# Performance work log

Hardware: AMD Instinct MI355X
Metric: run time of the kernel (lower is better)

## Reference

```python
import jax, jax.numpy as jnp
import numpy as np

LN_EPS = 1e-12
B, L, D, V, PATCH, IMG, C = 64, 40, 768, 30522, 16, 384, 3
GRID = IMG // PATCH            # 24
NPATCH = GRID * GRID           # 576


def layer_norm(x, g, b):
    m = jnp.mean(x, axis=-1, keepdims=True)
    v = jnp.var(x, axis=-1, keepdims=True)
    return (x - m) * jax.lax.rsqrt(v + LN_EPS) * g + b


def setup_inputs() -> dict:
    key = jax.random.key(0)
    ks = jax.random.split(key, 12)
    s = 0.02
    return {
        "input_ids": jax.random.randint(ks[0], (B, L), 0, V, dtype=jnp.int32),
        "attention_mask": jnp.ones((B, L), jnp.int32),
        "token_type_ids": jnp.zeros((B, L), jnp.int32),
        "pixel_values": jax.random.normal(ks[1], (B, C, IMG, IMG), jnp.float32),
        "pixel_mask": jnp.ones((B, IMG, IMG), jnp.int32),
        "word_emb": jax.random.normal(ks[2], (V, D), jnp.float32) * s,
        "text_pos_emb": jax.random.normal(ks[3], (L, D), jnp.float32) * s,
        "text_tok_emb": jax.random.normal(ks[4], (2, D), jnp.float32) * s,
        "ln_g": jnp.ones((D,), jnp.float32),
        "ln_b": jnp.zeros((D,), jnp.float32),
        "conv_w": jax.random.normal(ks[5], (D, C, PATCH, PATCH), jnp.float32) * s,
        "conv_b": jnp.zeros((D,), jnp.float32),
        "cls_token": jnp.zeros((1, 1, D), jnp.float32),
        "vis_pos_emb": jax.random.normal(ks[6], (1, NPATCH + 1, D), jnp.float32) * s,
        "mod_type_emb": jax.random.normal(ks[7], (2, D), jnp.float32) * s,
    }


def reference(input_ids, attention_mask, token_type_ids, pixel_values, pixel_mask,
              word_emb, text_pos_emb, text_tok_emb, ln_g, ln_b,
              conv_w, conv_b, cls_token, vis_pos_emb, mod_type_emb):
    # ---- text embeddings (BERT-style) ----
    te = word_emb[input_ids] + text_pos_emb[None, :, :] + text_tok_emb[token_type_ids]
    te = layer_norm(te, ln_g, ln_b)  # [B, L, D]

    # ---- visual_embed ----
    # patch projection conv (stride = patch size)
    x = jax.lax.conv_general_dilated(
        pixel_values, conv_w, window_strides=(PATCH, PATCH), padding='VALID',
        dimension_numbers=('NCHW', 'OIHW', 'NCHW')) + conv_b[None, :, None, None]
    # [B, D, 24, 24] -> [B, 576, D]
    x = x.reshape(B, D, NPATCH).transpose(0, 2, 1)
    # full pixel_mask => x_h = x_w = GRID for every sample; bilinear interp of the
    # [1, D, 24, 24] spatial pos-embed to (24, 24) with align_corners=True is identity,
    # all patches valid, valid_nums == max_image_length => selection is identity.
    pos_embed = vis_pos_emb[:, 1:, :]           # [1, NPATCH, D]
    img = x + pos_embed                          # [B, NPATCH, D]
    image_masks = jnp.ones((B, NPATCH), attention_mask.dtype)

    # ---- modality type embeddings ----
    te = te + mod_type_emb[0][None, None, :]
    img = img + mod_type_emb[1][None, None, :]

    # ---- concat with cls token ----
    emb = jnp.concatenate([te, img], axis=1)
    cls = jnp.broadcast_to(cls_token, (B, 1, D))
    emb = jnp.concatenate([cls, emb], axis=1)    # [B, 1+L+NPATCH, D]
    masks = jnp.concatenate(
        [jnp.ones((B, 1), attention_mask.dtype), attention_mask, image_masks], axis=1)
    return emb, masks
```

## Files before the change

kernel.cpp:

```cpp
#include <hip/hip_runtime.h>

typedef __attribute__((ext_vector_type(4))) float f4;
typedef __attribute__((ext_vector_type(4))) float f32x4;
typedef __attribute__((ext_vector_type(8))) __bf16 bf8;
typedef __attribute__((ext_vector_type(8))) unsigned short us8;

#define NB 64
#define LSEQ 40
#define D_DIM 768
#define NPATCH 576
#define SEQ 617
#define K_DIM 768
#define M_DIM (NB * NPATCH)
#define A_BYTES 56623104
#define GEMM_LDS 131072

static __device__ __forceinline__ unsigned short f2bf(float f) {
    union { float f; unsigned u; } v; v.f = f;
    unsigned r = v.u + 0x7FFFu + ((v.u >> 16) & 1u);
    return (unsigned short)(r >> 16);
}

static __device__ __forceinline__ void gload_lds16(const void* g, void* l) {
    __builtin_amdgcn_global_load_lds(
        (const __attribute__((address_space(1))) unsigned int*)g,
        (__attribute__((address_space(3))) unsigned int*)l,
        16, 0, 0);
}

__global__ __launch_bounds__(256) void convert_w(const float* __restrict__ w,
                                                 unsigned short* __restrict__ o) {
    int t = blockIdx.x * 256 + threadIdx.x;
    int cs = t % 96, n = t / 96;
    int blk = cs >> 3, c = cs & 7;
    int cl = (blk << 3) | (c ^ (n & 7));
    const float* s = w + (size_t)n * 768 + cl * 8;
    f4 a = *(const f4*)s;
    f4 b = *(const f4*)(s + 4);
    us8 r;
    r[0]=f2bf(a[0]); r[1]=f2bf(a[1]); r[2]=f2bf(a[2]); r[3]=f2bf(a[3]);
    r[4]=f2bf(b[0]); r[5]=f2bf(b[1]); r[6]=f2bf(b[2]); r[7]=f2bf(b[3]);
    *(us8*)(o + (size_t)n * 768 + cs * 8) = r;
}

__global__ __launch_bounds__(256) void convert_patches(const float* __restrict__ px,
                                                       unsigned short* __restrict__ A) {
    int t = blockIdx.x * 256 + threadIdx.x;
    int cs = t % 96, m = t / 96;
    int blk = cs >> 3, c = cs & 7;
    int cl = (blk << 3) | (c ^ (m & 7));
    int k = cl * 8;
    int b = m / 576, p = m % 576;
    int ph = p / 24, pw = p % 24;
    int ch = k >> 8, rr = k & 255, i = rr >> 4, j = rr & 15;
    const float* s = px + ((size_t)(b * 3 + ch) * 384 + ph * 16 + i) * 384 + pw * 16 + j;
    f4 a = *(const f4*)s;
    f4 d = *(const f4*)(s + 4);
    us8 o;
    o[0]=f2bf(a[0]); o[1]=f2bf(a[1]); o[2]=f2bf(a[2]); o[3]=f2bf(a[3]);
    o[4]=f2bf(d[0]); o[5]=f2bf(d[1]); o[6]=f2bf(d[2]); o[7]=f2bf(d[3]);
    *(us8*)(A + (size_t)m * 768 + cs * 8) = o;
}

__global__ __launch_bounds__(256) void text_kernel(
    const int* __restrict__ ids, const int* __restrict__ tti,
    const float* __restrict__ we, const float* __restrict__ pe,
    const float* __restrict__ tke, const float* __restrict__ g,
    const float* __restrict__ bb, const float* __restrict__ mod,
    float* __restrict__ out) {
    int row = blockIdx.x * 4 + (threadIdx.x >> 6);
    int lane = threadIdx.x & 63;
    int b = row / 40, l = row % 40;
    const float* wp = we + (size_t)ids[row] * 768;
    const float* pp = pe + l * 768;
    const float* tp = tke + (size_t)tti[row] * 768;
    f4 x[3];
    float s = 0.f, q = 0.f;
#pragma unroll
    for (int j = 0; j < 3; ++j) {
        int d = j * 256 + lane * 4;
        f4 v = *(const f4*)(wp + d);
        f4 v2 = *(const f4*)(pp + d);
        f4 v3 = *(const f4*)(tp + d);
        v = v + v2 + v3;
        x[j] = v;
        s += v[0] + v[1] + v[2] + v[3];
        q += v[0]*v[0] + v[1]*v[1] + v[2]*v[2] + v[3]*v[3];
    }
#pragma unroll
    for (int o = 32; o > 0; o >>= 1) { s += __shfl_xor(s, o); q += __shfl_xor(q, o); }
    float mean = s * (1.0f / 768.0f);
    float var = q * (1.0f / 768.0f) - mean * mean;
    float rstd = rsqrtf(var + 1e-12f);
    float* op = out + ((size_t)b * SEQ + 1 + l) * 768;
#pragma unroll
    for (int j = 0; j < 3; ++j) {
        int d = j * 256 + lane * 4;
        f4 gg = *(const f4*)(g + d);
        f4 bv = *(const f4*)(bb + d);
        f4 mm = *(const f4*)(mod + d);
        f4 r = (x[j] - mean) * rstd * gg + bv + mm;
        *(f4*)(op + d) = r;
    }
}

__global__ __launch_bounds__(512, 2) void gemm_patch(
    const __bf16* __restrict__ A, const __bf16* __restrict__ W,
    const float* __restrict__ conv_b, const float* __restrict__ vis_pos,
    const float* __restrict__ mod, float* __restrict__ out) {
    extern __shared__ __align__(16) char smem[];
    const int tid = threadIdx.x;
    const int w = tid >> 6, lane = tid & 63;

    int lid = blockIdx.x;
    int gwi = (lid & 7) * 54 + (lid >> 3);
    const int tile_n = (gwi % 3) * 256;
    const int tile_m = (gwi / 3) * 256;
    const int wm = w >> 2, wn = w & 3;
    const int wr = wm * 128, wc = wn * 64;

    f32x4 acc[8][4] = {};
    const char* Ab = (const char*)A;
    const char* Bb = (const char*)W;

    auto STAGE_A = [&](int p, int kt) {
        const int k0b = kt * 128;
        char* dst = smem + p * 32768;
#pragma unroll
        for (int i = 0; i < 4; ++i) {
            int uoff = (w << 10) + i * 8192;
            int loff = uoff + (lane << 4);
            int row = loff >> 7, col = loff & 127;
            gload_lds16(Ab + (size_t)(tile_m + row) * 1536 + k0b + col, dst + uoff);
        }
    };
    auto STAGE_B = [&](int p, int kt) {
        const int k0b = kt * 128;
        char* dst = smem + 65536 + p * 32768;
#pragma unroll
        for (int i = 0; i < 4; ++i) {
            int uoff = (w << 10) + i * 8192;
            int loff = uoff + (lane << 4);
            int row = loff >> 7, col = loff & 127;
            gload_lds16(Bb + (size_t)(tile_n + row) * 1536 + k0b + col, dst + uoff);
        }
    };

    STAGE_A(0, 0);
    STAGE_B(0, 0);
    asm volatile("s_waitcnt vmcnt(0)" ::: "memory");
    __builtin_amdgcn_sched_barrier(0);
    __builtin_amdgcn_s_barrier();
    __builtin_amdgcn_sched_barrier(0);

    const int rsel = lane & 15;
    const int hk = lane >> 4;

    for (int kt = 0; kt < 12; ++kt) {
        const int p = kt & 1;
        const char* Al = smem + p * 32768;
        const char* Bl = smem + 65536 + p * 32768;

        if (kt < 11) STAGE_A(p ^ 1, kt + 1);

        bf8 a0[4][2], b0[4][2];
#pragma unroll
        for (int mi = 0; mi < 4; ++mi) {
            int r = wr + mi * 16 + rsel;
#pragma unroll
            for (int ks = 0; ks < 2; ++ks) {
                int cst = (ks * 4 + hk) ^ (r & 7);
                a0[mi][ks] = *(const bf8*)(Al + r * 128 + cst * 16);
            }
        }
#pragma unroll
        for (int ni = 0; ni < 4; ++ni) {
            int r = wc + ni * 16 + rsel;
#pragma unroll
            for (int ks = 0; ks < 2; ++ks) {
                int cst = (ks * 4 + hk) ^ (r & 7);
                b0[ni][ks] = *(const bf8*)(Bl + r * 128 + cst * 16);
            }
        }

        if (kt < 11) STAGE_B(p ^ 1, kt + 1);

#pragma unroll
        for (int mi = 0; mi < 4; ++mi)
#pragma unroll
            for (int ni = 0; ni < 4; ++ni) {
                acc[mi][ni] = __builtin_amdgcn_mfma_f32_16x16x32_bf16(
                    a0[mi][0], b0[ni][0], acc[mi][ni], 0, 0, 0);
                acc[mi][ni] = __builtin_amdgcn_mfma_f32_16x16x32_bf16(
                    a0[mi][1], b0[ni][1], acc[mi][ni], 0, 0, 0);
            }

        bf8 a1[4][2];
#pragma unroll
        for (int mi = 0; mi < 4; ++mi) {
            int r = wr + 64 + mi * 16 + rsel;
#pragma unroll
            for (int ks = 0; ks < 2; ++ks) {
                int cst = (ks * 4 + hk) ^ (r & 7);
                a1[mi][ks] = *(const bf8*)(Al + r * 128 + cst * 16);
            }
        }
#pragma unroll
        for (int mi = 0; mi < 4; ++mi)
#pragma unroll
            for (int ni = 0; ni < 4; ++ni) {
                acc[4 + mi][ni] = __builtin_amdgcn_mfma_f32_16x16x32_bf16(
                    a1[mi][0], b0[ni][0], acc[4 + mi][ni], 0, 0, 0);
                acc[4 + mi][ni] = __builtin_amdgcn_mfma_f32_16x16x32_bf16(
                    a1[mi][1], b0[ni][1], acc[4 + mi][ni], 0, 0, 0);
            }

        if (kt < 11) {
            asm volatile("s_waitcnt vmcnt(0)" ::: "memory");
            __builtin_amdgcn_sched_barrier(0);
            __builtin_amdgcn_s_barrier();
            __builtin_amdgcn_sched_barrier(0);
        }
    }

    const int lr = (lane >> 4) * 4;
    const int lc = lane & 15;
#pragma unroll
    for (int mi = 0; mi < 8; ++mi) {
#pragma unroll
        for (int r = 0; r < 4; ++r) {
            int gm = tile_m + wr + mi * 16 + lr + r;
            int bimg = gm / 576, pp = gm % 576;
            size_t orow = (size_t)bimg * SEQ + 1 + LSEQ + pp;
#pragma unroll
            for (int ni = 0; ni < 4; ++ni) {
                int gn = tile_n + wc + ni * 16 + lc;
                float v = acc[mi][ni][r] + conv_b[gn] +
                          vis_pos[(size_t)(pp + 1) * 768 + gn] + mod[768 + gn];
                out[orow * 768 + gn] = v;
            }
        }
    }
}

__global__ __launch_bounds__(256) void cls_masks(const float* __restrict__ cls,
                                                 const int* __restrict__ am,
                                                 float* __restrict__ out) {
    int t = blockIdx.x * 256 + threadIdx.x;
    if (t < NB * 768) {
        int b = t / 768, d = t % 768;
        out[(size_t)b * SEQ * 768 + d] = cls[d];
    } else if (t < NB * 768 + NB * SEQ) {
        int i = t - NB * 768;
        int b = i / SEQ, s = i % SEQ;
        float v = 1.0f;
        if (s >= 1 && s <= LSEQ) v = (float)am[b * LSEQ + s - 1];
        out[(size_t)NB * SEQ * 768 + i] = v;
    }
}

extern "C" void kernel_launch(void* const* d_in, const int* in_sizes, int n_in,
                              void* d_out, int out_size, void* d_ws, size_t ws_size,
                              hipStream_t stream) {
    const int*   ids  = (const int*)d_in[0];
    const int*   am   = (const int*)d_in[1];
    const int*   tti  = (const int*)d_in[2];
    const float* px   = (const float*)d_in[3];
    const float* we   = (const float*)d_in[5];
    const float* pe   = (const float*)d_in[6];
    const float* tke  = (const float*)d_in[7];
    const float* lng  = (const float*)d_in[8];
    const float* lnb  = (const float*)d_in[9];
    const float* cw   = (const float*)d_in[10];
    const float* cb   = (const float*)d_in[11];
    const float* cls  = (const float*)d_in[12];
    const float* vpos = (const float*)d_in[13];
    const float* mod  = (const float*)d_in[14];
    float* out = (float*)d_out;

    __bf16* Abf = (__bf16*)d_ws;
    __bf16* Wbf = (__bf16*)((char*)d_ws + A_BYTES);

    hipFuncSetAttribute((const void*)gemm_patch,
                        hipFuncAttributeMaxDynamicSharedMemorySize, GEMM_LDS);

    convert_w<<<288, 256, 0, stream>>>(cw, (unsigned short*)Wbf);
    convert_patches<<<13824, 256, 0, stream>>>(px, (unsigned short*)Abf);
    text_kernel<<<640, 256, 0, stream>>>(ids, tti, we, pe, tke, lng, lnb, mod, out);
    gemm_patch<<<432, 512, GEMM_LDS, stream>>>(Abf, Wbf, cb, vpos, mod, out);
    cls_masks<<<347, 256, 0, stream>>>(cls, am, out);
}
```

Measured before the change: 108.2 us.

## Fuse patch extraction and bf16 conversion into GEMM A-tile loading

Drops the separate convert_patches kernel and its bf16 workspace. The GEMM now reads fp32 pixel rows straight from the image, converts them to bf16 in registers and writes them into swizzled LDS. This removes a full write and re-read of the 56MB patch matrix plus one launch. In exchange the kernel issues register-staged global loads and conversion ALU work per tile, and each A tile is re-read from the fp32 image by all three N-tiles.

New measurement: 101.5 us. 6.2% less time.

```diff
diff --git a/kernel.cpp b/kernel.cpp
--- a/kernel.cpp
+++ b/kernel.cpp
@@ -12,7 +12,6 @@
 #define SEQ 617
 #define K_DIM 768
 #define M_DIM (NB * NPATCH)
-#define A_BYTES 56623104
 #define GEMM_LDS 131072
 
 static __device__ __forceinline__ unsigned short f2bf(float f) {
@@ -27,6 +26,8 @@
         (__attribute__((address_space(3))) unsigned int*)l,
         16, 0, 0);
 }
+
+#define MFMA16(a, b, c) __builtin_amdgcn_mfma_f32_16x16x32_bf16((a), (b), (c), 0, 0, 0)
 
 __global__ __launch_bounds__(256) void convert_w(const float* __restrict__ w,
                                                  unsigned short* __restrict__ o) {
@@ -41,25 +42,6 @@
     r[0]=f2bf(a[0]); r[1]=f2bf(a[1]); r[2]=f2bf(a[2]); r[3]=f2bf(a[3]);
     r[4]=f2bf(b[0]); r[5]=f2bf(b[1]); r[6]=f2bf(b[2]); r[7]=f2bf(b[3]);
     *(us8*)(o + (size_t)n * 768 + cs * 8) = r;
-}
-
-__global__ __launch_bounds__(256) void convert_patches(const float* __restrict__ px,
-                                                       unsigned short* __restrict__ A) {
-    int t = blockIdx.x * 256 + threadIdx.x;
-    int cs = t % 96, m = t / 96;
-    int blk = cs >> 3, c = cs & 7;
-    int cl = (blk << 3) | (c ^ (m & 7));
-    int k = cl * 8;
-    int b = m / 576, p = m % 576;
-    int ph = p / 24, pw = p % 24;
-    int ch = k >> 8, rr = k & 255, i = rr >> 4, j = rr & 15;
-    const float* s = px + ((size_t)(b * 3 + ch) * 384 + ph * 16 + i) * 384 + pw * 16 + j;
-    f4 a = *(const f4*)s;
-    f4 d = *(const f4*)(s + 4);
-    us8 o;
-    o[0]=f2bf(a[0]); o[1]=f2bf(a[1]); o[2]=f2bf(a[2]); o[3]=f2bf(a[3]);
-    o[4]=f2bf(d[0]); o[5]=f2bf(d[1]); o[6]=f2bf(d[2]); o[7]=f2bf(d[3]);
-    *(us8*)(A + (size_t)m * 768 + cs * 8) = o;
 }
 
 __global__ __launch_bounds__(256) void text_kernel(
@@ -105,10 +87,15 @@
 }
 
 __global__ __launch_bounds__(512, 2) void gemm_patch(
-    const __bf16* __restrict__ A, const __bf16* __restrict__ W,
+    const float* __restrict__ px, const __bf16* __restrict__ W,
     const float* __restrict__ conv_b, const float* __restrict__ vis_pos,
     const float* __restrict__ mod, float* __restrict__ out) {
     extern __shared__ __align__(16) char smem[];
+    char* Ab0 = smem;
+    char* Ab1 = smem + 32768;
+    char* Bb0 = smem + 65536;
+    char* Bb1 = smem + 98304;
+
     const int tid = threadIdx.x;
     const int w = tid >> 6, lane = tid & 63;
 
@@ -120,48 +107,74 @@
     const int wr = wm * 128, wc = wn * 64;
 
     f32x4 acc[8][4] = {};
-    const char* Ab = (const char*)A;
     const char* Bb = (const char*)W;
-
-    auto STAGE_A = [&](int p, int kt) {
-        const int k0b = kt * 128;
-        char* dst = smem + p * 32768;
+    const int rsel = lane & 15;
+    const int hk = lane >> 4;
+
+    const int arow = tid & 255;
+    const int ii0 = tid >> 8;
+    {
+    }
+    int agm = tile_m + arow;
+    int abimg = agm / 576, ap = agm % 576;
+    int aph = ap / 24, apw = ap % 24;
+    const float* pxrow = px + (size_t)abimg * 3 * 147456
+                            + (size_t)(aph * 16) * 384 + apw * 16;
+
+    f4 areg[2][4];
+    auto LOAD_A = [&](int kt) {
+        int c = kt >> 2, i0 = (kt & 3) << 2;
+#pragma unroll
+        for (int rep = 0; rep < 2; ++rep) {
+            int i = i0 + ii0 + rep * 2;
+            const float* s = pxrow + (size_t)c * 147456 + i * 384;
+#pragma unroll
+            for (int q = 0; q < 4; ++q) areg[rep][q] = *(const f4*)(s + q * 4);
+        }
+    };
+    auto WRITE_A = [&](char* dst) {
+#pragma unroll
+        for (int rep = 0; rep < 2; ++rep) {
+            int ii = ii0 + rep * 2;
+            us8 h0, h1;
+#pragma unroll
+            for (int q = 0; q < 2; ++q) {
+                h0[q*4+0]=f2bf(areg[rep][q][0]); h0[q*4+1]=f2bf(areg[rep][q][1]);
+                h0[q*4+2]=f2bf(areg[rep][q][2]); h0[q*4+3]=f2bf(areg[rep][q][3]);
+                h1[q*4+0]=f2bf(areg[rep][q+2][0]); h1[q*4+1]=f2bf(areg[rep][q+2][1]);
+                h1[q*4+2]=f2bf(areg[rep][q+2][2]); h1[q*4+3]=f2bf(areg[rep][q+2][3]);
+            }
+            int cc0 = ii * 2;
+            *(us8*)(dst + arow * 128 + ((cc0    ) ^ (arow & 7)) * 16) = h0;
+            *(us8*)(dst + arow * 128 + ((cc0 + 1) ^ (arow & 7)) * 16) = h1;
+        }
+    };
+    auto STAGE_B = [&](char* lbase, int kt) {
 #pragma unroll
         for (int i = 0; i < 4; ++i) {
             int uoff = (w << 10) + i * 8192;
             int loff = uoff + (lane << 4);
             int row = loff >> 7, col = loff & 127;
-            gload_lds16(Ab + (size_t)(tile_m + row) * 1536 + k0b + col, dst + uoff);
+            gload_lds16(Bb + (size_t)(tile_n + row) * 1536 + kt * 128 + col,
+                        lbase + uoff);
         }
     };
-    auto STAGE_B = [&](int p, int kt) {
-        const int k0b = kt * 128;
-        char* dst = smem + 65536 + p * 32768;
-#pragma unroll
-        for (int i = 0; i < 4; ++i) {
-            int uoff = (w << 10) + i * 8192;
-            int loff = uoff + (lane << 4);
-            int row = loff >> 7, col = loff & 127;
-            gload_lds16(Bb + (size_t)(tile_n + row) * 1536 + k0b + col, dst + uoff);
-        }
-    };
-
-    STAGE_A(0, 0);
-    STAGE_B(0, 0);
-    asm volatile("s_waitcnt vmcnt(0)" ::: "memory");
-    __builtin_amdgcn_sched_barrier(0);
-    __builtin_amdgcn_s_barrier();
-    __builtin_amdgcn_sched_barrier(0);
-
-    const int rsel = lane & 15;
-    const int hk = lane >> 4;
-
-    for (int kt = 0; kt < 12; ++kt) {
-        const int p = kt & 1;
-        const char* Al = smem + p * 32768;
-        const char* Bl = smem + 65536 + p * 32768;
-
-        if (kt < 11) STAGE_A(p ^ 1, kt + 1);
+
+    LOAD_A(0);
+    STAGE_B(Bb0, 0);
+    WRITE_A(Ab0);
+    __syncthreads();
+
+    for (int t = 0; t < 12; ++t) {
+        char* Ac = (t & 1) ? Ab1 : Ab0;
+        char* Bc = (t & 1) ? Bb1 : Bb0;
+        char* An = (t & 1) ? Ab0 : Ab1;
+        char* Bn = (t & 1) ? Bb0 : Bb1;
+
+        if (t < 11) {
+            LOAD_A(t + 1);
+            STAGE_B(Bn, t + 1);
+        }
 
         bf8 a0[4][2], b0[4][2];
 #pragma unroll
@@ -170,7 +183,7 @@
 #pragma unroll
             for (int ks = 0; ks < 2; ++ks) {
                 int cst = (ks * 4 + hk) ^ (r & 7);
-                a0[mi][ks] = *(const bf8*)(Al + r * 128 + cst * 16);
+                a0[mi][ks] = *(const bf8*)(Ac + r * 128 + cst * 16);
             }
         }
 #pragma unroll
@@ -179,20 +192,15 @@
 #pragma unroll
             for (int ks = 0; ks < 2; ++ks) {
                 int cst = (ks * 4 + hk) ^ (r & 7);
-                b0[ni][ks] = *(const bf8*)(Bl + r * 128 + cst * 16);
-            }
-        }
-
-        if (kt < 11) STAGE_B(p ^ 1, kt + 1);
-
+                b0[ni][ks] = *(const bf8*)(Bc + r * 128 + cst * 16);
+            }
+        }
 #pragma unroll
         for (int mi = 0; mi < 4; ++mi)
 #pragma unroll
             for (int ni = 0; ni < 4; ++ni) {
-                acc[mi][ni] = __builtin_amdgcn_mfma_f32_16x16x32_bf16(
-                    a0[mi][0], b0[ni][0], acc[mi][ni], 0, 0, 0);
-                acc[mi][ni] = __builtin_amdgcn_mfma_f32_16x16x32_bf16(
-                    a0[mi][1], b0[ni][1], acc[mi][ni], 0, 0, 0);
+                acc[mi][ni] = MFMA16(a0[mi][0], b0[ni][0], acc[mi][ni]);
+                acc[mi][ni] = MFMA16(a0[mi][1], b0[ni][1], acc[mi][ni]);
             }
 
         bf8 a1[4][2];
@@ -202,24 +210,20 @@
 #pragma unroll
             for (int ks = 0; ks < 2; ++ks) {
                 int cst = (ks * 4 + hk) ^ (r & 7);
-                a1[mi][ks] = *(const bf8*)(Al + r * 128 + cst * 16);
+                a1[mi][ks] = *(const bf8*)(Ac + r * 128 + cst * 16);
             }
         }
 #pragma unroll
         for (int mi = 0; mi < 4; ++mi)
 #pragma unroll
             for (int ni = 0; ni < 4; ++ni) {
-                acc[4 + mi][ni] = __builtin_amdgcn_mfma_f32_16x16x32_bf16(
-                    a1[mi][0], b0[ni][0], acc[4 + mi][ni], 0, 0, 0);
-                acc[4 + mi][ni] = __builtin_amdgcn_mfma_f32_16x16x32_bf16(
-                    a1[mi][1], b0[ni][1], acc[4 + mi][ni], 0, 0, 0);
-            }
-
-        if (kt < 11) {
-            asm volatile("s_waitcnt vmcnt(0)" ::: "memory");
-            __builtin_amdgcn_sched_barrier(0);
-            __builtin_amdgcn_s_barrier();
-            __builtin_amdgcn_sched_barrier(0);
+                acc[4 + mi][ni] = MFMA16(a1[mi][0], b0[ni][0], acc[4 + mi][ni]);
+                acc[4 + mi][ni] = MFMA16(a1[mi][1], b0[ni][1], acc[4 + mi][ni]);
+            }
+
+        if (t < 11) {
+            WRITE_A(An);
+            __syncthreads();
         }
     }
 
@@ -230,13 +234,13 @@
 #pragma unroll
         for (int r = 0; r < 4; ++r) {
             int gm = tile_m + wr + mi * 16 + lr + r;
-            int bimg = gm / 576, pp = gm % 576;
-            size_t orow = (size_t)bimg * SEQ + 1 + LSEQ + pp;
+            int bimg = gm / 576, pp2 = gm % 576;
+            size_t orow = (size_t)bimg * SEQ + 1 + LSEQ + pp2;
 #pragma unroll
             for (int ni = 0; ni < 4; ++ni) {
                 int gn = tile_n + wc + ni * 16 + lc;
                 float v = acc[mi][ni][r] + conv_b[gn] +
-                          vis_pos[(size_t)(pp + 1) * 768 + gn] + mod[768 + gn];
+                          vis_pos[(size_t)(pp2 + 1) * 768 + gn] + mod[768 + gn];
                 out[orow * 768 + gn] = v;
             }
         }
@@ -278,15 +282,13 @@
     const float* mod  = (const float*)d_in[14];
     float* out = (float*)d_out;
 
-    __bf16* Abf = (__bf16*)d_ws;
-    __bf16* Wbf = (__bf16*)((char*)d_ws + A_BYTES);
+    __bf16* Wbf = (__bf16*)d_ws;
 
     hipFuncSetAttribute((const void*)gemm_patch,
                         hipFuncAttributeMaxDynamicSharedMemorySize, GEMM_LDS);
 
     convert_w<<<288, 256, 0, stream>>>(cw, (unsigned short*)Wbf);
-    convert_patches<<<13824, 256, 0, stream>>>(px, (unsigned short*)Abf);
     text_kernel<<<640, 256, 0, stream>>>(ids, tti, we, pe, tke, lng, lnb, mod, out);
-    gemm_patch<<<432, 512, GEMM_LDS, stream>>>(Abf, Wbf, cb, vpos, mod, out);
+    gemm_patch<<<432, 512, GEMM_LDS, stream>>>(px, Wbf, cb, vpos, mod, out);
     cls_masks<<<347, 256, 0, stream>>>(cls, am, out);
 }
```
